# Performance work log

Hardware: AMD Instinct MI355X
Metric: run time of the kernel (lower is better)

## Reference

```python
import jax, jax.numpy as jnp
import numpy as np

B, L2, N2, L1, N1 = 2, 4, 2048, 9, 8192
CIN, CT, CS, CORIG = 128, 128, 256, 64
R, STRIDE = 1, 2          # temporal_radius, temporal_stride; temporal_padding = [0, 0]
K = 2 * R + 1             # number of temporal MLPs
BN_EPS = 1e-5


def setup_inputs() -> dict:
    key = jax.random.key(0)
    ks = jax.random.split(key, 11)
    return {
        "xyzs": jax.random.normal(ks[0], (B, L2, N2, 3), jnp.float32),
        "original_xyzs": jax.random.normal(ks[1], (B, L1, N1, 3), jnp.float32),
        "features": jax.random.normal(ks[2], (B, L2, CIN, N2), jnp.float32),
        "original_features": jax.random.normal(ks[3], (B, L1, CORIG, N1), jnp.float32),
        # K temporal MLPs, each Conv1d(k=1): layer0 CIN->CT, layer1 CT->CT (bias=False)
        "Wt0": jax.random.normal(ks[4], (K, CT, CIN), jnp.float32) * 0.05,
        "Wt1": jax.random.normal(ks[5], (K, CT, CT), jnp.float32) * 0.05,
        # spatial Conv1d(k=1): (CT + CORIG) -> CS, then BN (eval mode) + ReLU
        "Ws": jax.random.normal(ks[6], (CS, CT + CORIG), jnp.float32) * 0.05,
        "bn_gamma": 1.0 + 0.1 * jax.random.normal(ks[7], (CS,), jnp.float32),
        "bn_beta": 0.1 * jax.random.normal(ks[8], (CS,), jnp.float32),
        "bn_mean": 0.1 * jax.random.normal(ks[9], (CS,), jnp.float32),
        "bn_var": jax.random.uniform(ks[10], (CS,), jnp.float32, 0.5, 1.5),
    }


def reference(xyzs, original_xyzs, features, original_features,
              Wt0, Wt1, Ws, bn_gamma, bn_beta, bn_mean, bn_var):
    # --- temporal MLPs: apply all K 1x1-conv stacks to every subsampled frame ---
    # h, tt: [B, L2, K, CT, N2]
    h = jax.nn.relu(jnp.einsum('koc,blcn->blkon', Wt0, features))
    tt = jax.nn.relu(jnp.einsum('koc,blkcn->blkon', Wt1, h))

    # middles / deltas (1-based frame indices, padding = [0,0])
    middles = [(t2 + 1) + t2 * (STRIDE - 1) + R for t2 in range(L2)]
    bn_scale = bn_gamma / jnp.sqrt(bn_var + BN_EPS)           # [CS]

    new_features = []
    for t1 in range(1, L1 + 1):
        seed_x, seed_f = [], []
        for t2 in range(L2):
            m = middles[t2]
            if m - R <= t1 <= m + R:
                seed_x.append(xyzs[:, t2])              # [B, N2, 3]
                seed_f.append(tt[:, t2, t1 - m + R])    # [B, CT, N2]
        sx = jnp.concatenate(seed_x, axis=1)            # [B, M, 3]
        sf = jnp.concatenate(seed_f, axis=2)            # [B, CT, M]
        ax = original_xyzs[:, t1 - 1]                   # [B, N1, 3]

        # three_nn: squared L2 dists, 3 nearest seeds per anchor point
        d2 = jnp.sum((ax[:, :, None, :] - sx[:, None, :, :]) ** 2, axis=-1)  # [B, N1, M]
        neg_d, idx = jax.lax.top_k(-d2, 3)              # [B, N1, 3]
        dist = -neg_d
        w = 1.0 / (dist + 1e-8)
        w = w / jnp.sum(w, axis=-1, keepdims=True)      # [B, N1, 3]

        # three_interpolate: gather 3 neighbor features per point and blend
        g = jnp.take_along_axis(sf[:, :, None, :], idx[:, None, :, :], axis=3)  # [B, CT, N1, 3]
        interp = jnp.sum(g * w[:, None, :, :], axis=-1)                         # [B, CT, N1]

        x = jnp.concatenate([interp, original_features[:, t1 - 1]], axis=1)     # [B, CT+CORIG, N1]
        x = jnp.einsum('oc,bcn->bon', Ws, x)                                     # [B, CS, N1]
        x = x * bn_scale[None, :, None] + (bn_beta - bn_mean * bn_scale)[None, :, None]
        new_features.append(jax.nn.relu(x))

    return original_xyzs, jnp.stack(new_features, axis=1)  # (B,L1,N1,3), (B,L1,CS,N1)
```

## Files before the change

### kernel.cpp

```cpp
#include <hip/hip_runtime.h>
#include <hip/hip_bf16.h>
#include <hip/hip_fp16.h>

#define BB 2
#define L2C 4
#define N2C 2048
#define L1C 9
#define N1C 8192
#define CINC 128
#define CTC 128
#define CSC 256
#define CORIGC 64
#define KC 3

#define OUT_XYZ_SIZE (BB*L1C*N1C*3)
#define FLT_BIG     3.402823466e38f

#define CHUNK   1024
#define GSTRIDE 20
#define NGROUPS 64
#define LDSF    (NGROUPS * GSTRIDE)

typedef __attribute__((ext_vector_type(8))) short bf16x8;
typedef __attribute__((ext_vector_type(4))) float f32x4;
typedef __attribute__((ext_vector_type(2))) float f32x2;
typedef __attribute__((ext_vector_type(4))) unsigned short u16x4;

#define MFMA16(a,b,c) __builtin_amdgcn_mfma_f32_16x16x32_bf16((a),(b),(c),0,0,0)

#define WS_TT_OFF   0
#define WS_NBR_OFF  12582912
#define WS_W_OFF    14352384
#define WS_BNP_OFF  14942208

__device__ __forceinline__ unsigned short bf16_hi(float v) {
    __hip_bfloat16 h = __float2bfloat16(v);
    return *(unsigned short*)&h;
}
__device__ __forceinline__ float bf16_to_f(unsigned short u) {
    unsigned int x = ((unsigned int)u) << 16;
    return __uint_as_float(x);
}

__device__ __forceinline__ f32x2 d2pk(f32x2 nx, f32x2 ny, f32x2 nz,
                                      f32x2 av0, f32x2 av1, f32x2 av2) {
    #pragma clang fp contract(off)
    f32x2 dx = av0 + nx;
    f32x2 dy = av1 + ny;
    f32x2 dz = av2 + nz;
    return (dx * dx + dy * dy) + dz * dz;
}

__global__ __launch_bounds__(256) void prep_kernel(const float* __restrict__ Wsm,
                                                   const float* __restrict__ Wt0,
                                                   const float* __restrict__ Wt1,
                                                   const float* __restrict__ gam,
                                                   const float* __restrict__ bet,
                                                   const float* __restrict__ mu,
                                                   const float* __restrict__ var,
                                                   unsigned short* __restrict__ WsH,
                                                   unsigned short* __restrict__ WsL,
                                                   unsigned short* __restrict__ W0H,
                                                   unsigned short* __restrict__ W0L,
                                                   unsigned short* __restrict__ W1H,
                                                   unsigned short* __restrict__ W1L,
                                                   float* __restrict__ bnp) {
    for (int i = blockIdx.x * 256 + threadIdx.x; i < 49152; i += gridDim.x * 256) {
        float a = Wsm[i]; unsigned short h = bf16_hi(a);
        WsH[i] = h; WsL[i] = bf16_hi(a - bf16_to_f(h));
        float b = Wt0[i]; h = bf16_hi(b);
        W0H[i] = h; W0L[i] = bf16_hi(b - bf16_to_f(h));
        float c = Wt1[i]; h = bf16_hi(c);
        W1H[i] = h; W1L[i] = bf16_hi(c - bf16_to_f(h));
    }
    if (blockIdx.x == 0) {
        int o = threadIdx.x;
        float sc = gam[o] / sqrtf(var[o] + 1e-5f);
        bnp[o]       = sc;
        bnp[CSC + o] = bet[o] - mu[o] * sc;
    }
}

__global__ __launch_bounds__(256) void tt_kernel(const float* __restrict__ feat,
                                                 const unsigned short* __restrict__ W0H,
                                                 const unsigned short* __restrict__ W0L,
                                                 const unsigned short* __restrict__ W1H,
                                                 const unsigned short* __restrict__ W1L,
                                                 unsigned short* __restrict__ tt) {
    __shared__ unsigned short Bh[16 * 64 * 8];
    __shared__ unsigned short Bl[16 * 64 * 8];
    __shared__ unsigned short Hh[16 * 64 * 8];
    const int t     = threadIdx.x;
    const int slice = blockIdx.y;
    const int k     = blockIdx.z;
    const int n0    = blockIdx.x * 64;
    const int lane  = t & 63;
    const int w     = t >> 6;
    const int l15   = lane & 15;
    const int quad  = lane >> 4;

    const float* f = feat + (size_t)slice * CINC * N2C;
    for (int i = 0; i < 32; ++i) {
        int idx = i * 256 + t;
        int c = idx >> 6, n = idx & 63;
        float v = f[(size_t)c * N2C + n0 + n];
        unsigned short h = bf16_hi(v);
        int bi = (((c >> 3) * 64) + n) * 8 + (c & 7);
        Bh[bi] = h;
        Bl[bi] = bf16_hi(v - bf16_to_f(h));
    }
    __syncthreads();

    unsigned short* ttg = tt + (size_t)slice * KC * N2C * CTC;
    const f32x4 zero = {0.f, 0.f, 0.f, 0.f};

    f32x4 acc[2][4];
    for (int oi = 0; oi < 2; ++oi)
        for (int ni = 0; ni < 4; ++ni) acc[oi][ni] = zero;
    {
        const unsigned short* AH = W0H + (size_t)k * CTC * CINC;
        const unsigned short* AL = W0L + (size_t)k * CTC * CINC;
        for (int kst = 0; kst < 4; ++kst) {
            bf16x8 ah[2], al[2], bh[4], bl[4];
            #pragma unroll
            for (int oi = 0; oi < 2; ++oi) {
                int o = 32 * w + oi * 16 + l15;
                ah[oi] = *(const bf16x8*)(AH + (size_t)o * CINC + kst * 32 + quad * 8);
                al[oi] = *(const bf16x8*)(AL + (size_t)o * CINC + kst * 32 + quad * 8);
            }
            #pragma unroll
            for (int ni = 0; ni < 4; ++ni) {
                int n = ni * 16 + l15;
                int c8 = kst * 4 + quad;
                bh[ni] = *(const bf16x8*)&Bh[(c8 * 64 + n) * 8];
                bl[ni] = *(const bf16x8*)&Bl[(c8 * 64 + n) * 8];
            }
            #pragma unroll
            for (int oi = 0; oi < 2; ++oi)
                #pragma unroll
                for (int ni = 0; ni < 4; ++ni) {
                    acc[oi][ni] = MFMA16(ah[oi], bh[ni], acc[oi][ni]);
                    acc[oi][ni] = MFMA16(ah[oi], bl[ni], acc[oi][ni]);
                    acc[oi][ni] = MFMA16(al[oi], bh[ni], acc[oi][ni]);
                }
        }
    }
    #pragma unroll
    for (int oi = 0; oi < 2; ++oi)
        #pragma unroll
        for (int ni = 0; ni < 4; ++ni) {
            int n = ni * 16 + l15;
            int obase = 32 * w + oi * 16 + quad * 4;
            int ch = obase >> 3, jj = obase & 7;
            unsigned short* dst = &Hh[(ch * 64 + n) * 8 + jj];
            dst[0] = bf16_hi(fmaxf(acc[oi][ni][0], 0.f));
            dst[1] = bf16_hi(fmaxf(acc[oi][ni][1], 0.f));
            dst[2] = bf16_hi(fmaxf(acc[oi][ni][2], 0.f));
            dst[3] = bf16_hi(fmaxf(acc[oi][ni][3], 0.f));
        }
    __syncthreads();

    f32x4 acc2[2][4];
    for (int oi = 0; oi < 2; ++oi)
        for (int ni = 0; ni < 4; ++ni) acc2[oi][ni] = zero;
    {
        const unsigned short* AH = W1H + (size_t)k * CTC * CTC;
        const unsigned short* AL = W1L + (size_t)k * CTC * CTC;
        for (int kst = 0; kst < 4; ++kst) {
            bf16x8 ah[2], al[2], bh[4];
            #pragma unroll
            for (int oi = 0; oi < 2; ++oi) {
                int o = 32 * w + oi * 16 + l15;
                ah[oi] = *(const bf16x8*)(AH + (size_t)o * CTC + kst * 32 + quad * 8);
                al[oi] = *(const bf16x8*)(AL + (size_t)o * CTC + kst * 32 + quad * 8);
            }
            #pragma unroll
            for (int ni = 0; ni < 4; ++ni) {
                int n = ni * 16 + l15;
                int c8 = kst * 4 + quad;
                bh[ni] = *(const bf16x8*)&Hh[(c8 * 64 + n) * 8];
            }
            #pragma unroll
            for (int oi = 0; oi < 2; ++oi)
                #pragma unroll
                for (int ni = 0; ni < 4; ++ni) {
                    acc2[oi][ni] = MFMA16(ah[oi], bh[ni], acc2[oi][ni]);
                    acc2[oi][ni] = MFMA16(al[oi], bh[ni], acc2[oi][ni]);
                }
        }
    }
    #pragma unroll
    for (int oi = 0; oi < 2; ++oi)
        #pragma unroll
        for (int ni = 0; ni < 4; ++ni) {
            int n2 = n0 + ni * 16 + l15;
            int obase = 32 * w + oi * 16 + quad * 4;
            u16x4 vv;
            vv[0] = bf16_hi(fmaxf(acc2[oi][ni][0], 0.f));
            vv[1] = bf16_hi(fmaxf(acc2[oi][ni][1], 0.f));
            vv[2] = bf16_hi(fmaxf(acc2[oi][ni][2], 0.f));
            vv[3] = bf16_hi(fmaxf(acc2[oi][ni][3], 0.f));
            *(u16x4*)&ttg[((size_t)k * N2C + n2) * CTC + obase] = vv;
        }
}

__global__ __launch_bounds__(256, 8) void knn_kernel(const float* __restrict__ xyzs,
                                                     const float* __restrict__ oxyz,
                                                     unsigned int* __restrict__ nbr) {
    __shared__ __align__(16) float sx[LDSF];
    __shared__ __align__(16) float sy[LDSF];
    __shared__ __align__(16) float sz[LDSF];
    float* candd = sx;
    int*   candi = (int*)sy;
    const int t   = threadIdx.x;
    const int bt1 = blockIdx.y;
    const int b   = bt1 / L1C;
    const int t1  = bt1 % L1C + 1;
    int t2min = (t1 - 2) >> 1; if (t2min < 0) t2min = 0;
    int t2max = (t1 - 1) >> 1; if (t2max > 3) t2max = 3;
    const int S = (t2max - t2min + 1) * N2C;

    const int a  = t & 63;
    const int p  = t >> 6;
    const int n1 = blockIdx.x * 64 + a;
    const float* ap = oxyz + ((size_t)bt1 * N1C + n1) * 3;
    const float ax = ap[0], ay = ap[1], az = ap[2];
    const f32x2 ax2 = {ax, ax}, ay2 = {ay, ay}, az2 = {az, az};

    float b0 = FLT_BIG, b1 = FLT_BIG, b2 = FLT_BIG;
    int   i0 = 0, i1 = 0, i2 = 0;

    for (int cb = 0; cb < S; cb += CHUNK) {
        if (cb) __syncthreads();
        {
            int t2  = t2min + (cb >> 11);
            int off = cb & (N2C - 1);
            const float* base = xyzs + ((size_t)(b * L2C + t2) * N2C + off) * 3;
            for (int s = t; s < CHUNK; s += 256) {
                const float* pp = base + (size_t)s * 3;
                int li = (s >> 4) * GSTRIDE + (s & 15);
                sx[li] = -pp[0]; sy[li] = -pp[1]; sz[li] = -pp[2];
            }
        }
        __syncthreads();

        const int g0i = p * 16;

        float gm0 = FLT_BIG, gm1 = FLT_BIG, gm2 = FLT_BIG;
        int   gs0 = g0i << 4, gs1 = g0i << 4, gs2 = g0i << 4;
        for (int g = g0i; g < g0i + 16; ++g) {
            const int gb = g * GSTRIDE;
            f32x2 dd[8];
            #pragma unroll
            for (int q = 0; q < 4; ++q) {
                float4 X = ((const float4*)&sx[gb])[q];
                float4 Y = ((const float4*)&sy[gb])[q];
                float4 Z = ((const float4*)&sz[gb])[q];
                f32x2 xlo = {X.x, X.y}, xhi = {X.z, X.w};
                f32x2 ylo = {Y.x, Y.y}, yhi = {Y.z, Y.w};
                f32x2 zlo = {Z.x, Z.y}, zhi = {Z.z, Z.w};
                dd[2 * q]     = d2pk(xlo, ylo, zlo, ax2, ay2, az2);
                dd[2 * q + 1] = d2pk(xhi, yhi, zhi, ax2, ay2, az2);
            }
            float e0 = fminf(dd[0][0], dd[0][1]);
            float e1 = fminf(dd[1][0], dd[1][1]);
            float e2 = fminf(dd[2][0], dd[2][1]);
            float e3 = fminf(dd[3][0], dd[3][1]);
            float e4 = fminf(dd[4][0], dd[4][1]);
            float e5 = fminf(dd[5][0], dd[5][1]);
            float e6 = fminf(dd[6][0], dd[6][1]);
            float e7 = fminf(dd[7][0], dd[7][1]);
            float f0 = fminf(e0, e1), f1 = fminf(e2, e3);
            float f2 = fminf(e4, e5), f3 = fminf(e6, e7);
            float m  = fminf(fminf(f0, f1), fminf(f2, f3));
            int sb = g << 4;
            bool c0 = m < gm0, c1 = m < gm1, c2 = m < gm2;
            int ns0 = c0 ? sb  : gs0;
            int ns1 = c0 ? gs0 : (c1 ? sb : gs1);
            int ns2 = c1 ? gs1 : (c2 ? sb : gs2);
            float nm0 = fminf(gm0, m);
            float nm1 = __builtin_amdgcn_fmed3f(gm0, gm1, m);
            float nm2 = __builtin_amdgcn_fmed3f(gm1, gm2, m);
            gm0 = nm0; gm1 = nm1; gm2 = nm2;
            gs0 = ns0; gs1 = ns1; gs2 = ns2;
        }

        int lo01 = min(gs0, gs1), hi01 = max(gs0, gs1);
        int gA = min(lo01, gs2);
        int gC = max(hi01, gs2);
        int gB = (gs0 + gs1 + gs2) - gA - gC;

        #pragma unroll
        for (int v = 0; v < 3; ++v) {
            int sb = (v == 0) ? gA : ((v == 1) ? gB : gC);
            const int lb = (sb >> 4) * GSTRIDE;
            f32x2 dd[8];
            #pragma unroll
            for (int q = 0; q < 4; ++q) {
                float4 X = ((const float4*)&sx[lb])[q];
                float4 Y = ((const float4*)&sy[lb])[q];
                float4 Z = ((const float4*)&sz[lb])[q];
                f32x2 xlo = {X.x, X.y}, xhi = {X.z, X.w};
                f32x2 ylo = {Y.x, Y.y}, yhi = {Y.z, Y.w};
                f32x2 zlo = {Z.x, Z.y}, zhi = {Z.z, Z.w};
                dd[2 * q]     = d2pk(xlo, ylo, zlo, ax2, ay2, az2);
                dd[2 * q + 1] = d2pk(xhi, yhi, zhi, ax2, ay2, az2);
            }
            #pragma unroll
            for (int jp = 0; jp < 8; ++jp)
                #pragma unroll
                for (int h = 0; h < 2; ++h) {
                    float d = dd[jp][h];
                    int   s = cb + sb + jp * 2 + h;
                    bool c0 = d < b0, c1 = d < b1, c2 = d < b2;
                    int ni0 = c0 ? s  : i0;
                    int ni1 = c0 ? i0 : (c1 ? s : i1);
                    int ni2 = c1 ? i1 : (c2 ? s : i2);
                    float nb0 = fminf(b0, d);
                    float nb1 = __builtin_amdgcn_fmed3f(b0, b1, d);
                    float nb2 = __builtin_amdgcn_fmed3f(b1, b2, d);
                    b0 = nb0; b1 = nb1; b2 = nb2;
                    i0 = ni0; i1 = ni1; i2 = ni2;
                }
        }
    }
    __syncthreads();

    candd[(a * 4 + p) * 3 + 0] = b0; candi[(a * 4 + p) * 3 + 0] = i0;
    candd[(a * 4 + p) * 3 + 1] = b1; candi[(a * 4 + p) * 3 + 1] = i1;
    candd[(a * 4 + p) * 3 + 2] = b2; candi[(a * 4 + p) * 3 + 2] = i2;
    __syncthreads();

    if (t < 64) {
        float dd[12]; int ii[12];
        for (int q = 0; q < 12; ++q) { dd[q] = candd[t * 12 + q]; ii[q] = candi[t * 12 + q]; }
        for (int x = 1; x < 12; ++x) {
            float dv = dd[x]; int iv = ii[x]; int y = x - 1;
            while (y >= 0 && (dd[y] > dv || (dd[y] == dv && ii[y] > iv))) {
                dd[y + 1] = dd[y]; ii[y + 1] = ii[y]; --y;
            }
            dd[y + 1] = dv; ii[y + 1] = iv;
        }
        float w0 = 1.f / (dd[0] + 1e-8f);
        float w1 = 1.f / (dd[1] + 1e-8f);
        float w2 = 1.f / (dd[2] + 1e-8f);
        float wsum = (w0 + w1) + w2;
        float wv[3] = { w0 / wsum, w1 / wsum, w2 / wsum };
        size_t base = ((size_t)bt1 * N1C + blockIdx.x * 64 + t) * 3;
        #pragma unroll
        for (int j = 0; j < 3; ++j) {
            int s  = ii[j];
            int t2 = t2min + (s >> 11);
            int n2 = s & 2047;
            int kidx = t1 - 2 * t2 - 1;
            unsigned int idx16 = (unsigned int)(((b * L2C + t2) * KC + kidx) * N2C + n2);
            unsigned short hb = __half_as_ushort(__float2half(wv[j]));
            nbr[base + j] = (idx16 << 16) | (unsigned int)hb;
        }
    }
}

__global__ __launch_bounds__(256) void out_kernel(const float* __restrict__ ofeat,
                                                  const unsigned short* __restrict__ WsH,
                                                  const unsigned short* __restrict__ WsL,
                                                  const unsigned short* __restrict__ tt,
                                                  const unsigned int* __restrict__ nbr,
                                                  const float* __restrict__ bnp,
                                                  float* __restrict__ out) {
    __shared__ unsigned short xh[24 * 64 * 8];
    __shared__ unsigned short xl[24 * 64 * 8];
    const int t    = threadIdx.x;
    const int bt1  = blockIdx.y;
    const int n0   = blockIdx.x * 64;
    const int w    = t >> 6;
    const int lane = t & 63;

    const int c0 = 2 * lane;
    for (int nn = 0; nn < 16; ++nn) {
        int n = w * 16 + nn;
        size_t kb = ((size_t)bt1 * N1C + n0 + n) * 3;
        unsigned int u0 = nbr[kb], u1 = nbr[kb + 1], u2 = nbr[kb + 2];
        const unsigned short* p0 = tt + (size_t)(u0 >> 16) * CTC;
        const unsigned short* p1 = tt + (size_t)(u1 >> 16) * CTC;
        const unsigned short* p2 = tt + (size_t)(u2 >> 16) * CTC;
        float q0 = __half2float(__ushort_as_half((unsigned short)(u0 & 0xffffu)));
        float q1 = __half2float(__ushort_as_half((unsigned short)(u1 & 0xffffu)));
        float q2 = __half2float(__ushort_as_half((unsigned short)(u2 & 0xffffu)));
        unsigned int g0 = *(const unsigned int*)(p0 + c0);
        unsigned int g1 = *(const unsigned int*)(p1 + c0);
        unsigned int g2 = *(const unsigned int*)(p2 + c0);
        float vE = (bf16_to_f((unsigned short)(g0 & 0xffffu)) * q0
                  + bf16_to_f((unsigned short)(g1 & 0xffffu)) * q1)
                  + bf16_to_f((unsigned short)(g2 & 0xffffu)) * q2;
        float vO = (bf16_to_f((unsigned short)(g0 >> 16)) * q0
                  + bf16_to_f((unsigned short)(g1 >> 16)) * q1)
                  + bf16_to_f((unsigned short)(g2 >> 16)) * q2;
        int bi = (((c0 >> 3) * 64) + n) * 8 + (c0 & 7);
        unsigned short hE = bf16_hi(vE), hO = bf16_hi(vO);
        *(unsigned int*)&xh[bi] = (unsigned int)hE | ((unsigned int)hO << 16);
        unsigned short lE = bf16_hi(vE - bf16_to_f(hE));
        unsigned short lO = bf16_hi(vO - bf16_to_f(hO));
        *(unsigned int*)&xl[bi] = (unsigned int)lE | ((unsigned int)lO << 16);
    }
    {
        const float* ofp = ofeat + (size_t)bt1 * CORIGC * N1C;
        for (int i = 0; i < 16; ++i) {
            int idx = i * 256 + t;
            int cp = idx >> 6, n = idx & 63;
            float v = ofp[(size_t)cp * N1C + n0 + n];
            int c = CTC + cp;
            int bi = (((c >> 3) * 64) + n) * 8 + (c & 7);
            unsigned short h = bf16_hi(v);
            xh[bi] = h; xl[bi] = bf16_hi(v - bf16_to_f(h));
        }
    }
    __syncthreads();

    const int l15  = lane & 15;
    const int quad = lane >> 4;
    const f32x4 zero = {0.f, 0.f, 0.f, 0.f};
    f32x4 acc[4][4];
    for (int mi = 0; mi < 4; ++mi)
        for (int oi = 0; oi < 4; ++oi) acc[mi][oi] = zero;

    for (int kst = 0; kst < 6; ++kst) {
        bf16x8 ah[4], al[4], bh[4], bl[4];
        #pragma unroll
        for (int mi = 0; mi < 4; ++mi) {
            int n = mi * 16 + l15;
            int c8 = kst * 4 + quad;
            ah[mi] = *(const bf16x8*)&xh[(c8 * 64 + n) * 8];
            al[mi] = *(const bf16x8*)&xl[(c8 * 64 + n) * 8];
        }
        #pragma unroll
        for (int oi = 0; oi < 4; ++oi) {
            int o = w * 64 + oi * 16 + l15;
            bh[oi] = *(const bf16x8*)(WsH + (size_t)o * 192 + kst * 32 + quad * 8);
            bl[oi] = *(const bf16x8*)(WsL + (size_t)o * 192 + kst * 32 + quad * 8);
        }
        #pragma unroll
        for (int mi = 0; mi < 4; ++mi)
            #pragma unroll
            for (int oi = 0; oi < 4; ++oi) {
                acc[mi][oi] = MFMA16(ah[mi], bh[oi], acc[mi][oi]);
                acc[mi][oi] = MFMA16(ah[mi], bl[oi], acc[mi][oi]);
                acc[mi][oi] = MFMA16(al[mi], bh[oi], acc[mi][oi]);
            }
    }

    float* outp = out + OUT_XYZ_SIZE + (size_t)bt1 * CSC * N1C;
    #pragma unroll
    for (int oi = 0; oi < 4; ++oi) {
        int o = w * 64 + oi * 16 + l15;
        float sc = bnp[o], sh = bnp[CSC + o];
        #pragma unroll
        for (int mi = 0; mi < 4; ++mi) {
            int nb = n0 + mi * 16 + quad * 4;
            f32x4 y;
            y[0] = fmaxf(acc[mi][oi][0] * sc + sh, 0.f);
            y[1] = fmaxf(acc[mi][oi][1] * sc + sh, 0.f);
            y[2] = fmaxf(acc[mi][oi][2] * sc + sh, 0.f);
            y[3] = fmaxf(acc[mi][oi][3] * sc + sh, 0.f);
            *(f32x4*)&outp[(size_t)o * N1C + nb] = y;
        }
    }
}

extern "C" void kernel_launch(void* const* d_in, const int* in_sizes, int n_in,
                              void* d_out, int out_size, void* d_ws, size_t ws_size,
                              hipStream_t stream) {
    const float* xyzs  = (const float*)d_in[0];
    const float* oxyz  = (const float*)d_in[1];
    const float* feat  = (const float*)d_in[2];
    const float* ofeat = (const float*)d_in[3];
    const float* Wt0   = (const float*)d_in[4];
    const float* Wt1   = (const float*)d_in[5];
    const float* Wsm   = (const float*)d_in[6];
    const float* gam   = (const float*)d_in[7];
    const float* bet   = (const float*)d_in[8];
    const float* mu    = (const float*)d_in[9];
    const float* var   = (const float*)d_in[10];
    float* out = (float*)d_out;
    char*  wsb = (char*)d_ws;

    unsigned short* tt  = (unsigned short*)(wsb + WS_TT_OFF);
    unsigned int*   nbr = (unsigned int*)(wsb + WS_NBR_OFF);
    unsigned short* WsH = (unsigned short*)(wsb + WS_W_OFF);
    unsigned short* WsL = WsH + 49152;
    unsigned short* W0H = WsL + 49152;
    unsigned short* W0L = W0H + 49152;
    unsigned short* W1H = W0L + 49152;
    unsigned short* W1L = W1H + 49152;
    float*          bnp = (float*)(wsb + WS_BNP_OFF);

    hipMemcpyAsync(out, oxyz, (size_t)OUT_XYZ_SIZE * sizeof(float),
                   hipMemcpyDeviceToDevice, stream);

    hipLaunchKernelGGL(prep_kernel, dim3(64), dim3(256), 0, stream,
                       Wsm, Wt0, Wt1, gam, bet, mu, var,
                       WsH, WsL, W0H, W0L, W1H, W1L, bnp);
    hipLaunchKernelGGL(tt_kernel, dim3(32, BB * L2C, KC), dim3(256), 0, stream,
                       feat, W0H, W0L, W1H, W1L, tt);
    hipLaunchKernelGGL(knn_kernel, dim3(128, BB * L1C), dim3(256), 0, stream,
                       xyzs, oxyz, nbr);
    hipLaunchKernelGGL(out_kernel, dim3(128, BB * L1C), dim3(256), 0, stream,
                       ofeat, WsH, WsL, tt, nbr, bnp, out);
}
```

Baseline: 468.4 us.

## Split out_kernel GEMM into two LDS phases to shrink shared memory

The output kernel now runs the GEMM over the interpolated features (first 128 channels) first, then reuses the same smaller LDS buffer for the 64 original-feature channels and finishes the K loop. LDS per block drops from 24 to 16 channel-groups, and launch bounds request 5 blocks per CU, with the aim of raising occupancy. The cost is an extra barrier pair and serialization between the interpolation gather and the original-feature load, and the launch-bounds hint may force register spilling of the 16 accumulators.

```diff
diff --git a/kernel.cpp b/kernel.cpp
--- a/kernel.cpp
+++ b/kernel.cpp
@@ -360,20 +360,27 @@
     }
 }
 
-__global__ __launch_bounds__(256) void out_kernel(const float* __restrict__ ofeat,
-                                                  const unsigned short* __restrict__ WsH,
-                                                  const unsigned short* __restrict__ WsL,
-                                                  const unsigned short* __restrict__ tt,
-                                                  const unsigned int* __restrict__ nbr,
-                                                  const float* __restrict__ bnp,
-                                                  float* __restrict__ out) {
-    __shared__ unsigned short xh[24 * 64 * 8];
-    __shared__ unsigned short xl[24 * 64 * 8];
+__global__ __launch_bounds__(256, 5) void out_kernel(const float* __restrict__ ofeat,
+                                                     const unsigned short* __restrict__ WsH,
+                                                     const unsigned short* __restrict__ WsL,
+                                                     const unsigned short* __restrict__ tt,
+                                                     const unsigned int* __restrict__ nbr,
+                                                     const float* __restrict__ bnp,
+                                                     float* __restrict__ out) {
+    __shared__ unsigned short xh[16 * 64 * 8];
+    __shared__ unsigned short xl[16 * 64 * 8];
     const int t    = threadIdx.x;
     const int bt1  = blockIdx.y;
     const int n0   = blockIdx.x * 64;
     const int w    = t >> 6;
     const int lane = t & 63;
+    const int l15  = lane & 15;
+    const int quad = lane >> 4;
+
+    const f32x4 zero = {0.f, 0.f, 0.f, 0.f};
+    f32x4 acc[4][4];
+    for (int mi = 0; mi < 4; ++mi)
+        for (int oi = 0; oi < 4; ++oi) acc[mi][oi] = zero;
 
     const int c0 = 2 * lane;
     for (int nn = 0; nn < 16; ++nn) {
@@ -402,35 +409,55 @@
         unsigned short lO = bf16_hi(vO - bf16_to_f(hO));
         *(unsigned int*)&xl[bi] = (unsigned int)lE | ((unsigned int)lO << 16);
     }
+    __syncthreads();
+
+    for (int kst = 0; kst < 4; ++kst) {
+        bf16x8 ah[4], al[4], bh[4], bl[4];
+        #pragma unroll
+        for (int mi = 0; mi < 4; ++mi) {
+            int n = mi * 16 + l15;
+            int c8 = kst * 4 + quad;
+            ah[mi] = *(const bf16x8*)&xh[(c8 * 64 + n) * 8];
+            al[mi] = *(const bf16x8*)&xl[(c8 * 64 + n) * 8];
+        }
+        #pragma unroll
+        for (int oi = 0; oi < 4; ++oi) {
+            int o = w * 64 + oi * 16 + l15;
+            bh[oi] = *(const bf16x8*)(WsH + (size_t)o * 192 + kst * 32 + quad * 8);
+            bl[oi] = *(const bf16x8*)(WsL + (size_t)o * 192 + kst * 32 + quad * 8);
+        }
+        #pragma unroll
+        for (int mi = 0; mi < 4; ++mi)
+            #pragma unroll
+            for (int oi = 0; oi < 4; ++oi) {
+                acc[mi][oi] = MFMA16(ah[mi], bh[oi], acc[mi][oi]);
+                acc[mi][oi] = MFMA16(ah[mi], bl[oi], acc[mi][oi]);
+                acc[mi][oi] = MFMA16(al[mi], bh[oi], acc[mi][oi]);
+            }
+    }
+    __syncthreads();
+
     {
         const float* ofp = ofeat + (size_t)bt1 * CORIGC * N1C;
         for (int i = 0; i < 16; ++i) {
             int idx = i * 256 + t;
             int cp = idx >> 6, n = idx & 63;
             float v = ofp[(size_t)cp * N1C + n0 + n];
-            int c = CTC + cp;
-            int bi = (((c >> 3) * 64) + n) * 8 + (c & 7);
+            int bi = (((cp >> 3) * 64) + n) * 8 + (cp & 7);
             unsigned short h = bf16_hi(v);
             xh[bi] = h; xl[bi] = bf16_hi(v - bf16_to_f(h));
         }
     }
     __syncthreads();
 
-    const int l15  = lane & 15;
-    const int quad = lane >> 4;
-    const f32x4 zero = {0.f, 0.f, 0.f, 0.f};
-    f32x4 acc[4][4];
-    for (int mi = 0; mi < 4; ++mi)
-        for (int oi = 0; oi < 4; ++oi) acc[mi][oi] = zero;
-
-    for (int kst = 0; kst < 6; ++kst) {
+    for (int kst = 4; kst < 6; ++kst) {
         bf16x8 ah[4], al[4], bh[4], bl[4];
         #pragma unroll
         for (int mi = 0; mi < 4; ++mi) {
             int n = mi * 16 + l15;
-            int c8 = kst * 4 + quad;
-            ah[mi] = *(const bf16x8*)&xh[(c8 * 64 + n) * 8];
-            al[mi] = *(const bf16x8*)&xl[(c8 * 64 + n) * 8];
+            int c8p = (kst - 4) * 4 + quad;
+            ah[mi] = *(const bf16x8*)&xh[(c8p * 64 + n) * 8];
+            al[mi] = *(const bf16x8*)&xl[(c8p * 64 + n) * 8];
         }
         #pragma unroll
         for (int oi = 0; oi < 4; ++oi) {
```

New measurement: 631.3 us. 1.35x slower.
